# Optimization experiments

Hardware: AMD Instinct MI355X
Metric: run time of the kernel (lower is better)

## Reference

```python
import jax, jax.numpy as jnp
import numpy as np

TEMPERATURE = 0.1  # from __init__ temperature
NEG_INF = -1e30


def setup_inputs() -> dict:
    key = jax.random.key(0)
    k1, k2, k3, k4, k5 = jax.random.split(key, 5)
    B, D = 8192, 128
    return {
        "zis": jax.random.normal(k1, (B, D), dtype=jnp.float32),
        "zjs": jax.random.normal(k2, (B, D), dtype=jnp.float32),
        "ilabels": jax.random.randint(k3, (B,), 0, 100, dtype=jnp.int64),
        "jlabels": jax.random.randint(k4, (B,), 0, 100, dtype=jnp.int64),
        "weights": jax.random.uniform(k5, (B,), dtype=jnp.float32),
        "idx": 0,
    }


def reference(zis, zjs, ilabels, jlabels, weights, idx):
    B = zjs.shape[0]
    # forward F.normalize + cosine_matrix's normalize is idempotent -> single L2 normalize
    zi = zis / jnp.linalg.norm(zis, axis=1, keepdims=True)
    zj = zjs / jnp.linalg.norm(zjs, axis=1, keepdims=True)
    # similarity_matrix = 1 - (1 - zj @ zi^T); rows indexed by zjs
    logits = (zj @ zi.T) / TEMPERATURE  # [B, B]
    # labels[i, j] = (ilabels[j] == jlabels[i])
    labels = ilabels[None, :] == jlabels[:, None]  # [B, B] bool
    neg_mask = ~labels  # 'zeros' columns per row
    rows = jnp.arange(B)
    pos_idx = idx + rows  # class_level=False: ones = idx + i, size = 1
    pos = logits[rows, pos_idx]  # [B]
    # CrossEntropy over cat([pos, logits[i, zeros]]) at label 0:
    # loss_i = logsumexp([pos_i, neg_row_i]) - pos_i (numerically stable)
    neg_max = jnp.max(jnp.where(neg_mask, logits, NEG_INF), axis=1)
    m = jnp.maximum(pos, neg_max)  # [B]
    denom = jnp.exp(pos - m) + jnp.sum(
        jnp.where(neg_mask, jnp.exp(logits - m[:, None]), 0.0), axis=1
    )
    loss = m + jnp.log(denom) - pos  # [B]
    # size==1 path: loss*w / w (faithful to torch weighted sum / weight.sum())
    w = weights[pos_idx]
    loss = (loss * w) / w
    return jnp.sum(loss) / B
```

## Files before the change

### kernel.cpp

```cpp
#include <hip/hip_runtime.h>


#define BB 8192
#define DD 128
#define CP 256
#define RSL 512
#define NGR 16

typedef __attribute__((ext_vector_type(8))) short short8;
typedef __attribute__((ext_vector_type(4))) float floatx4;

#define GLOBAL_AS __attribute__((address_space(1)))
#define LDS_AS    __attribute__((address_space(3)))

#define L2E10 14.4269504088896340f

static __device__ __forceinline__ float wave_sum(float v) {
#pragma unroll
    for (int off = 32; off > 0; off >>= 1) v += __shfl_xor(v, off, 64);
    return v;
}

static __device__ __forceinline__ unsigned short f2bf(float f) {
    unsigned int u = __float_as_uint(f);
    return (unsigned short)((u + 0x7FFFu + ((u >> 16) & 1u)) >> 16);
}

__global__ __launch_bounds__(256) void prep_kernel(
    const float* __restrict__ zis, const float* __restrict__ zjs,
    unsigned short* __restrict__ Zib, unsigned short* __restrict__ Zjb,
    float* __restrict__ rni, float* __restrict__ rnj,
    float* __restrict__ denom, float* __restrict__ out, int nout)
{
    if (threadIdx.x < 2) denom[blockIdx.x * 2 + threadIdx.x] = 0.0f;
    if (blockIdx.x == 0 && (int)threadIdx.x < nout) out[threadIdx.x] = 0.0f;

    int wave = threadIdx.x >> 6, lane = threadIdx.x & 63;
    int row = blockIdx.x * 4 + wave;
    const float* src; unsigned short* dst; float* rn; int r;
    if (row < BB) { src = zis; dst = Zib; rn = rni; r = row; }
    else          { src = zjs; dst = Zjb; rn = rnj; r = row - BB; }
    float2 u = *(const float2*)(src + (size_t)r * DD + lane * 2);
    float s = wave_sum(u.x * u.x + u.y * u.y);
    float sc = 1.0f / sqrtf(s);
    if (lane == 0) rn[r] = sc;
    ushort2 o; o.x = f2bf(u.x * sc); o.y = f2bf(u.y * sc);
    *(ushort2*)(dst + (size_t)r * DD + lane * 2) = o;
}

__global__ __launch_bounds__(512, 2) void panel_kernel(
    const unsigned short* __restrict__ Zjb,
    const unsigned short* __restrict__ Zib,
    const int* __restrict__ ilab, const int* __restrict__ jlab,
    float* __restrict__ denom)
{
    __shared__ __align__(16) unsigned short Bp[CP * DD];
    __shared__ int Il[CP];

    int tid  = threadIdx.x;
    int lane = tid & 63, wave = tid >> 6;
    int quad = lane >> 4, l15 = lane & 15;
    int c0    = blockIdx.y * CP;
    int rbase = blockIdx.x * RSL;

    {
        int nl = wave * 4 + quad;
        int s  = l15 ^ (nl & 15);
        const unsigned short* gp0 = Zib + (size_t)(c0 + nl) * DD + s * 8;
#pragma unroll
        for (int u = 0; u < 8; ++u) {
            const unsigned short* gp = gp0 + (size_t)u * 32 * DD;
            unsigned short* lp = &Bp[(u * 8 + wave) * 512];
            __builtin_amdgcn_global_load_lds((const GLOBAL_AS void*)gp,
                                             (LDS_AS void*)lp, 16, 0, 0);
        }
    }
    if (tid < CP) Il[tid] = ilab[c0 + tid];
    asm volatile("s_waitcnt vmcnt(0) lgkmcnt(0)" ::: "memory");
    __builtin_amdgcn_s_barrier();

    const unsigned short* rb0 = &Bp[l15 * DD + (((0 * 4 + quad) ^ l15) * 8)];
    const unsigned short* rb1 = &Bp[l15 * DD + (((1 * 4 + quad) ^ l15) * 8)];
    const unsigned short* rb2 = &Bp[l15 * DD + (((2 * 4 + quad) ^ l15) * 8)];
    const unsigned short* rb3 = &Bp[l15 * DD + (((3 * 4 + quad) ^ l15) * 8)];
    const int* ilb = &Il[l15];

#define LDB(bx, g) do {                                       \
        bx[0] = *(const short8*)(rb0 + (g) * 16 * DD);        \
        bx[1] = *(const short8*)(rb1 + (g) * 16 * DD);        \
        bx[2] = *(const short8*)(rb2 + (g) * 16 * DD);        \
        bx[3] = *(const short8*)(rb3 + (g) * 16 * DD);        \
    } while (0)

#define MFMA8(bx) do {                                                          \
        floatx4 zz = (floatx4){0.f, 0.f, 0.f, 0.f};                             \
        acc[0] = __builtin_amdgcn_mfma_f32_16x16x32_bf16(af[0][0], bx[0], zz, 0, 0, 0); \
        acc[1] = __builtin_amdgcn_mfma_f32_16x16x32_bf16(af[1][0], bx[0], zz, 0, 0, 0); \
        acc[0] = __builtin_amdgcn_mfma_f32_16x16x32_bf16(af[0][1], bx[1], acc[0], 0, 0, 0); \
        acc[1] = __builtin_amdgcn_mfma_f32_16x16x32_bf16(af[1][1], bx[1], acc[1], 0, 0, 0); \
        acc[0] = __builtin_amdgcn_mfma_f32_16x16x32_bf16(af[0][2], bx[2], acc[0], 0, 0, 0); \
        acc[1] = __builtin_amdgcn_mfma_f32_16x16x32_bf16(af[1][2], bx[2], acc[1], 0, 0, 0); \
        acc[0] = __builtin_amdgcn_mfma_f32_16x16x32_bf16(af[0][3], bx[3], acc[0], 0, 0, 0); \
        acc[1] = __builtin_amdgcn_mfma_f32_16x16x32_bf16(af[1][3], bx[3], acc[1], 0, 0, 0); \
    } while (0)

#define EPI(ilc) do {                                         \
        _Pragma("unroll")                                     \
        for (int mt = 0; mt < 2; ++mt)                        \
            _Pragma("unroll")                                 \
            for (int r = 0; r < 4; ++r) {                     \
                float e = __builtin_amdgcn_exp2f(             \
                    fmaf(acc[mt][r], L2E10, -L2E10));         \
                rs[mt][r] += ((ilc) != jrv[mt * 4 + r]) ? e : 0.0f; \
            }                                                 \
    } while (0)

#pragma unroll
    for (int c = 0; c < 2; ++c) {
        int r0 = rbase + wave * 64 + c * 32;

        short8 af[2][4];
#pragma unroll
        for (int mt = 0; mt < 2; ++mt)
#pragma unroll
            for (int ks = 0; ks < 4; ++ks)
                af[mt][ks] = *(const short8*)(Zjb
                    + (size_t)(r0 + mt * 16 + l15) * DD + ks * 32 + quad * 8);

        int jrv[8];
#pragma unroll
        for (int mt = 0; mt < 2; ++mt)
#pragma unroll
            for (int r = 0; r < 4; ++r)
                jrv[mt * 4 + r] = jlab[r0 + mt * 16 + quad * 4 + r];

        float rs[2][4];
#pragma unroll
        for (int mt = 0; mt < 2; ++mt)
#pragma unroll
            for (int r = 0; r < 4; ++r) rs[mt][r] = 0.0f;

        floatx4 acc[2];
        short8 b0[4], b1[4];
        LDB(b0, 0);
        int iln = ilb[0];

        __builtin_amdgcn_s_setprio(1);
#pragma unroll
        for (int g = 0; g < NGR; g += 2) {
            LDB(b1, g + 1);
            int il0 = iln; iln = ilb[(g + 1) * 16];
            MFMA8(b0);
            EPI(il0);
            if (g + 2 < NGR) LDB(b0, g + 2);
            int il1 = iln;
            if (g + 2 < NGR) iln = ilb[(g + 2) * 16];
            MFMA8(b1);
            EPI(il1);
        }
        __builtin_amdgcn_s_setprio(0);

#pragma unroll
        for (int mt = 0; mt < 2; ++mt)
#pragma unroll
            for (int r = 0; r < 4; ++r) {
                float v = rs[mt][r];
                v += __shfl_xor(v, 1, 64);
                v += __shfl_xor(v, 2, 64);
                v += __shfl_xor(v, 4, 64);
                v += __shfl_xor(v, 8, 64);
                if (l15 == 0)
                    atomicAdd(&denom[r0 + mt * 16 + quad * 4 + r], v);
            }
    }
#undef LDB
#undef MFMA8
#undef EPI
}

__global__ __launch_bounds__(256) void posfinal_kernel(
    const float* __restrict__ zis, const float* __restrict__ zjs,
    const float* __restrict__ rni, const float* __restrict__ rnj,
    const float* __restrict__ denom, const float* __restrict__ wts,
    const int* __restrict__ idxp, float* __restrict__ out)
{
    int wave = threadIdx.x >> 6, lane = threadIdx.x & 63;
    int idx = idxp[0];
    float ll = 0.0f;
#pragma unroll
    for (int t = 0; t < 4; ++t) {
        int i = blockIdx.x * 16 + wave * 4 + t;
        int j = idx + i;
        float2 a  = *(const float2*)(zjs + (size_t)i * DD + lane * 2);
        float2 b2 = *(const float2*)(zis + (size_t)j * DD + lane * 2);
        float s = wave_sum(a.x * b2.x + a.y * b2.y);
        if (lane == 0) {
            float p = s * rni[j] * rnj[i] * 10.0f;
            float l = 10.0f + logf(__expf(p - 10.0f) + denom[i]) - p;
            float w = wts[j];
            ll += (l * w) / w;
        }
    }
    __shared__ float part[4];
    if (lane == 0) part[wave] = ll;
    __syncthreads();
    if (threadIdx.x == 0)
        atomicAdd(out, (part[0] + part[1] + part[2] + part[3]) * (1.0f / BB));
}

extern "C" void kernel_launch(void* const* d_in, const int* in_sizes, int n_in,
                              void* d_out, int out_size, void* d_ws, size_t ws_size,
                              hipStream_t stream) {
    const float* zis = (const float*)d_in[0];
    const float* zjs = (const float*)d_in[1];
    const int* ilab = (const int*)d_in[2];
    const int* jlab = (const int*)d_in[3];
    const float* wts = (const float*)d_in[4];
    const int* idxp = (const int*)d_in[5];
    float* out = (float*)d_out;

    float* rni   = (float*)d_ws;
    float* rnj   = rni + BB;
    float* denom = rnj + BB;
    unsigned short* Zib = (unsigned short*)(denom + BB);
    unsigned short* Zjb = Zib + (size_t)BB * DD;

    prep_kernel<<<2 * BB / 4, 256, 0, stream>>>(
        zis, zjs, Zib, Zjb, rni, rnj, denom, out, out_size);
    panel_kernel<<<dim3(BB / RSL, BB / CP), 512, 0, stream>>>(
        Zjb, Zib, ilab, jlab, denom);
    posfinal_kernel<<<BB / 16, 256, 0, stream>>>(
        zis, zjs, rni, rnj, denom, wts, idxp, out);
}
```

Baseline: 109.8 us.

## Fuse positive-logit and final loss reduction into panel kernel via last-block tickets

Removes the separate posfinal launch. Each panel block bumps a per-row-slab ticket counter after its denominator atomics. The last of the 32 column blocks for a slab then computes the positive logits, the per-row losses and the weighted sum for its 512 rows. This saves a kernel launch and a grid-wide dependency, but the tail work is now done by only 16 blocks, each walking 64 serial iterations with atomics. There is also no explicit memory fence before taking the ticket.

```diff
diff --git a/kernel.cpp b/kernel.cpp
--- a/kernel.cpp
+++ b/kernel.cpp
@@ -30,10 +30,12 @@
     const float* __restrict__ zis, const float* __restrict__ zjs,
     unsigned short* __restrict__ Zib, unsigned short* __restrict__ Zjb,
     float* __restrict__ rni, float* __restrict__ rnj,
-    float* __restrict__ denom, float* __restrict__ out, int nout)
+    float* __restrict__ denom, int* __restrict__ tickets,
+    float* __restrict__ out, int nout)
 {
     if (threadIdx.x < 2) denom[blockIdx.x * 2 + threadIdx.x] = 0.0f;
     if (blockIdx.x == 0 && (int)threadIdx.x < nout) out[threadIdx.x] = 0.0f;
+    if (blockIdx.x == 1 && threadIdx.x < 16) tickets[threadIdx.x] = 0;
 
     int wave = threadIdx.x >> 6, lane = threadIdx.x & 63;
     int row = blockIdx.x * 4 + wave;
@@ -52,10 +54,16 @@
     const unsigned short* __restrict__ Zjb,
     const unsigned short* __restrict__ Zib,
     const int* __restrict__ ilab, const int* __restrict__ jlab,
-    float* __restrict__ denom)
+    float* __restrict__ denom, int* __restrict__ tickets,
+    const float* __restrict__ zis, const float* __restrict__ zjs,
+    const float* __restrict__ rni, const float* __restrict__ rnj,
+    const float* __restrict__ wts, const int* __restrict__ idxp,
+    float* __restrict__ out)
 {
     __shared__ __align__(16) unsigned short Bp[CP * DD];
     __shared__ int Il[CP];
+    __shared__ float part[8];
+    __shared__ int tkt;
 
     int tid  = threadIdx.x;
     int lane = tid & 63, wave = tid >> 6;
@@ -176,36 +184,36 @@
 #undef LDB
 #undef MFMA8
 #undef EPI
-}
-
-__global__ __launch_bounds__(256) void posfinal_kernel(
-    const float* __restrict__ zis, const float* __restrict__ zjs,
-    const float* __restrict__ rni, const float* __restrict__ rnj,
-    const float* __restrict__ denom, const float* __restrict__ wts,
-    const int* __restrict__ idxp, float* __restrict__ out)
-{
-    int wave = threadIdx.x >> 6, lane = threadIdx.x & 63;
-    int idx = idxp[0];
-    float ll = 0.0f;
-#pragma unroll
-    for (int t = 0; t < 4; ++t) {
-        int i = blockIdx.x * 16 + wave * 4 + t;
-        int j = idx + i;
-        float2 a  = *(const float2*)(zjs + (size_t)i * DD + lane * 2);
-        float2 b2 = *(const float2*)(zis + (size_t)j * DD + lane * 2);
-        float s = wave_sum(a.x * b2.x + a.y * b2.y);
-        if (lane == 0) {
-            float p = s * rni[j] * rnj[i] * 10.0f;
-            float l = 10.0f + logf(__expf(p - 10.0f) + denom[i]) - p;
-            float w = wts[j];
-            ll += (l * w) / w;
+
+    __syncthreads();
+    if (tid == 0) tkt = atomicAdd(&tickets[blockIdx.x], 1);
+    __syncthreads();
+    if (tkt == 31) {
+        int idx2 = idxp[0];
+        float ll = 0.0f;
+        for (int t = 0; t < RSL / (8 * 64) * 64; ++t) {
+            int i = rbase + wave * 64 + t;
+            int j = idx2 + i;
+            float2 a  = *(const float2*)(zjs + (size_t)i * DD + lane * 2);
+            float2 b2 = *(const float2*)(zis + (size_t)j * DD + lane * 2);
+            float s = wave_sum(a.x * b2.x + a.y * b2.y);
+            if (lane == 0) {
+                float d = atomicAdd(&denom[i], 0.0f);
+                float p = s * rni[j] * rnj[i] * 10.0f;
+                float l = 10.0f + logf(__expf(p - 10.0f) + d) - p;
+                float w = wts[j];
+                ll += (l * w) / w;
+            }
+        }
+        if (lane == 0) part[wave] = ll;
+        __syncthreads();
+        if (tid == 0) {
+            float sum = 0.0f;
+#pragma unroll
+            for (int q = 0; q < 8; ++q) sum += part[q];
+            atomicAdd(out, sum * (1.0f / BB));
         }
     }
-    __shared__ float part[4];
-    if (lane == 0) part[wave] = ll;
-    __syncthreads();
-    if (threadIdx.x == 0)
-        atomicAdd(out, (part[0] + part[1] + part[2] + part[3]) * (1.0f / BB));
 }
 
 extern "C" void kernel_launch(void* const* d_in, const int* in_sizes, int n_in,
@@ -222,13 +230,13 @@
     float* rni   = (float*)d_ws;
     float* rnj   = rni + BB;
     float* denom = rnj + BB;
-    unsigned short* Zib = (unsigned short*)(denom + BB);
+    int*   tickets = (int*)(denom + BB);
+    unsigned short* Zib = (unsigned short*)(tickets + 64);
     unsigned short* Zjb = Zib + (size_t)BB * DD;
 
     prep_kernel<<<2 * BB / 4, 256, 0, stream>>>(
-        zis, zjs, Zib, Zjb, rni, rnj, denom, out, out_size);
+        zis, zjs, Zib, Zjb, rni, rnj, denom, tickets, out, out_size);
     panel_kernel<<<dim3(BB / RSL, BB / CP), 512, 0, stream>>>(
-        Zjb, Zib, ilab, jlab, denom);
-    posfinal_kernel<<<BB / 16, 256, 0, stream>>>(
-        zis, zjs, rni, rnj, denom, wts, idxp, out);
-}
+        Zjb, Zib, ilab, jlab, denom, tickets,
+        zis, zjs, rni, rnj, wts, idxp, out);
+}
```

After: 165.3 us. +50.5%, slower.
